# Optimization experiments

Hardware: AMD Instinct MI355X
Metric: run time of the kernel (lower is better)

## Reference

```python
import jax, jax.numpy as jnp
import numpy as np

B, T, NE, NH, HD = 4, 1024, 768, 12, 64
CURV = 0.0
EPS = 1e-6
LN_EPS = 1e-5
ROPE_BASE = 10000.0


def project(x, k):
    # Lift Euclidean vector onto Lorentz hyperboloid with curvature K = exp(k):
    # time coord t = sqrt(K + ||x||^2) so that <lx, lx>_L = -K.
    K = jnp.exp(k)
    t = jnp.sqrt(K + jnp.sum(x * x, axis=-1, keepdims=True))
    return jnp.concatenate([t, x], axis=-1)


def lorentz_distance(lq, lk, k):
    # lq, lk: (B, H, T, D+1); k: (1, H, 1, 1) log-curvature.
    # d = sqrt(K) * arccosh(clamp(-<q,k>_L / K, 1+eps))
    K = jnp.exp(k)
    inner = (jnp.einsum('bhid,bhjd->bhij', lq[..., 1:], lk[..., 1:])
             - jnp.einsum('bhi,bhj->bhij', lq[..., 0], lk[..., 0]))
    c = jnp.clip(-inner / K, 1.0 + EPS, None)
    return jnp.sqrt(K) * jnp.arccosh(c)


def lorentz_norm(x):
    # sqrt(|<x,x>_L|) with <x,x>_L = -x0^2 + ||xs||^2  (keepdim)
    inner = -x[..., 0:1] ** 2 + jnp.sum(x[..., 1:] ** 2, axis=-1, keepdims=True)
    return jnp.sqrt(jnp.clip(-inner, EPS, None))


def rotary_tables():
    inv_freq = 1.0 / (ROPE_BASE ** (np.arange(0, HD, 2, dtype=np.float32) / HD))
    t = np.arange(T, dtype=np.float32)
    freqs = np.outer(t, inv_freq)  # (T, HD/2)
    cos = jnp.asarray(np.cos(freqs))[None, :, None, :]  # (1,T,1,HD/2)
    sin = jnp.asarray(np.sin(freqs))[None, :, None, :]
    return cos, sin


def apply_rotary(x, cos, sin):
    # x: (B, T, H, HD)
    x1, x2 = x[..., : HD // 2], x[..., HD // 2:]
    return jnp.concatenate([x1 * cos + x2 * sin, -x1 * sin + x2 * cos], axis=-1)


def layernorm(y, g, b):
    m = jnp.mean(y, axis=-1, keepdims=True)
    v = jnp.mean((y - m) ** 2, axis=-1, keepdims=True)
    return (y - m) / jnp.sqrt(v + LN_EPS) * g + b


def setup_inputs() -> dict:
    key = jax.random.key(0)
    ks = jax.random.split(key, 8)
    s = 0.02
    return {
        'x': jax.random.normal(ks[0], (B, T, NE), dtype=jnp.float32),
        'block_curvature': jnp.asarray(CURV, dtype=jnp.float32),
        'mlp_curvature': jnp.asarray(CURV, dtype=jnp.float32),
        'attn_curvatures': jnp.ones((1, NH, 1, 1), dtype=jnp.float32) * CURV,
        'qkv_w': jax.random.normal(ks[1], (3 * NE, NE + 1), dtype=jnp.float32) * s,
        'attn_proj_w': jax.random.normal(ks[2], (NE, (HD + 1) * NH), dtype=jnp.float32) * s,
        'attn_proj_b': jnp.zeros((NE,), dtype=jnp.float32),
        'mlp_expand_w': jax.random.normal(ks[3], (4 * NE + 3, NE + 1), dtype=jnp.float32) * s,
        'mlp_expand_b': jnp.zeros((4 * NE + 3,), dtype=jnp.float32),
        'mlp_shrink_w': jax.random.normal(ks[4], (NE, 4 * (NE + 1)), dtype=jnp.float32) * s,
        'mlp_shrink_b': jnp.zeros((NE,), dtype=jnp.float32),
        'ln_g': jnp.ones((NE,), dtype=jnp.float32),
        'ln_b': jnp.zeros((NE,), dtype=jnp.float32),
    }


def reference(x, block_curvature, mlp_curvature, attn_curvatures, qkv_w,
              attn_proj_w, attn_proj_b, mlp_expand_w, mlp_expand_b,
              mlp_shrink_w, mlp_shrink_b, ln_g, ln_b):
    cos, sin = rotary_tables()
    causal_bias = jnp.where(
        jnp.triu(jnp.ones((T, T), dtype=bool), k=1), -jnp.inf, 0.0).astype(jnp.float32)

    def block_norm(lx):
        return project(layernorm(lx[..., 1:], ln_g, ln_b), block_curvature)

    def attn(lx):
        qkv = lx @ qkv_w.T  # (B, T, 3*NE)
        q, k, v = jnp.split(qkv, 3, axis=-1)
        q = apply_rotary(q.reshape(B, T, NH, HD), cos, sin)
        k = apply_rotary(k.reshape(B, T, NH, HD), cos, sin)
        v = v.reshape(B, T, NH, HD)
        lq = project(q.transpose(0, 2, 1, 3), attn_curvatures)  # (B,H,T,HD+1)
        lk = project(k.transpose(0, 2, 1, 3), attn_curvatures)
        lv = project(v.transpose(0, 2, 1, 3), attn_curvatures)
        dis = lorentz_distance(lq, lk, attn_curvatures)  # (B,H,T,T)
        aw = jax.nn.softmax(-dis + causal_bias, axis=-1)
        a = jnp.einsum('bhij,bhjd->bhid', aw, lv)  # (B,H,T,HD+1)
        a = a * jnp.sqrt(jnp.exp(attn_curvatures)) / lorentz_norm(a)
        a = a.transpose(0, 2, 1, 3).reshape(B, T, NH * (HD + 1))
        a = a @ attn_proj_w.T + attn_proj_b
        return project(a, block_curvature)

    def mlp(lx):
        h = lx @ mlp_expand_w.T + mlp_expand_b  # (B,T,4*NE+3)
        h = project(h, mlp_curvature)[..., 1:]  # drop time coord back to 4*NE+3
        h = jax.nn.gelu(h, approximate=False)
        h = project(h, mlp_curvature)  # (B,T,4*(NE+1))
        h = h @ mlp_shrink_w.T + mlp_shrink_b
        return project(h, block_curvature)

    def skip(lx, f_lx):
        return project(lx[..., 1:] + f_lx[..., 1:], block_curvature)

    lx = project(x, block_curvature)  # (B,T,NE+1)
    lx = skip(lx, attn(block_norm(lx)))
    lx = skip(lx, mlp(block_norm(lx)))
    return lx
```

## Files before the change

kernel.cpp:

```cpp
#include <hip/hip_runtime.h>
#include <cmath>

typedef unsigned short ushort_t;
typedef __attribute__((ext_vector_type(8))) short short8;
typedef __attribute__((ext_vector_type(4))) float floatx4;

#define NH    12
#define T     1024
#define ROWS  4096
#define NE    768
#define KPA   800
#define KPB   3104
#define NEXP  3200
#define HEXP  3075
#define NSPLIT 2

__device__ __forceinline__ ushort_t f2bf(float f) {
  union { float f; unsigned u; } v; v.f = f;
  unsigned r = v.u + 0x7fffu + ((v.u >> 16) & 1u);
  return (ushort_t)(r >> 16);
}
__device__ __forceinline__ float bf2f(ushort_t b) {
  union { unsigned u; float f; } v; v.u = ((unsigned)b) << 16;
  return v.f;
}
__device__ __forceinline__ float blk_reduce_sum(float v, float* sm) {
  #pragma unroll
  for (int o = 32; o > 0; o >>= 1) v += __shfl_xor(v, o, 64);
  int lane = threadIdx.x & 63, w = threadIdx.x >> 6;
  __syncthreads();
  if (lane == 0) sm[w] = v;
  __syncthreads();
  return sm[0] + sm[1] + sm[2] + sm[3];
}
__device__ __forceinline__ float red16_sum(float v) {
  #pragma unroll
  for (int o = 1; o < 16; o <<= 1) v += __shfl_xor(v, o, 64);
  return v;
}
__device__ __forceinline__ float red16_max(float v) {
  #pragma unroll
  for (int o = 1; o < 16; o <<= 1) v = fmaxf(v, __shfl_xor(v, o, 64));
  return v;
}

#define NB_A 7200
#define NB_B 2400
#define NB_C 10000
#define NB_D 9312
#define NB_E 16
__device__ __forceinline__ void cvt_elem(ushort_t* __restrict__ dst,
                                         const float* __restrict__ src,
                                         int idx, int srcRows, int srcK, int dstK) {
  int r = idx / dstK, c = idx - r * dstK;
  dst[idx] = (r < srcRows && c < srcK) ? f2bf(src[(size_t)r * srcK + c]) : (ushort_t)0;
}
__global__ __launch_bounds__(256) void prep_kernel(
    ushort_t* __restrict__ qkv_wb, const float* __restrict__ qkvw,
    ushort_t* __restrict__ proj_wb, const float* __restrict__ projw,
    ushort_t* __restrict__ exp_wb, const float* __restrict__ expw,
    ushort_t* __restrict__ shr_wb, const float* __restrict__ shrw,
    ushort_t* __restrict__ aout_bf) {
  int blk = blockIdx.x;
  int tid = threadIdx.x;
  if (blk < NB_A) {
    cvt_elem(qkv_wb, qkvw, blk * 256 + tid, 2304, 769, KPA);
  } else if (blk < NB_A + NB_B) {
    cvt_elem(proj_wb, projw, (blk - NB_A) * 256 + tid, 768, 780, KPA);
  } else if (blk < NB_A + NB_B + NB_C) {
    cvt_elem(exp_wb, expw, (blk - NB_A - NB_B) * 256 + tid, HEXP, 769, KPA);
  } else if (blk < NB_A + NB_B + NB_C + NB_D) {
    cvt_elem(shr_wb, shrw, (blk - NB_A - NB_B - NB_C) * 256 + tid, 768, 3076, KPB);
  } else {
    int r = (blk - NB_A - NB_B - NB_C - NB_D) * 256 + tid;
    ushort_t* p = aout_bf + (size_t)r * KPA + 780;
    #pragma unroll
    for (int j = 0; j < 20; ++j) p[j] = 0;
  }
}

__global__ __launch_bounds__(256) void ln_project(
    const float* __restrict__ xin, const float* __restrict__ g,
    const float* __restrict__ bb, const float* __restrict__ curv,
    ushort_t* __restrict__ outp) {
  __shared__ float sm[4];
  const int row = blockIdx.x;
  const int tid = threadIdx.x;
  const float* xr = xin + (size_t)row * NE;
  float xv[3];
  float s = 0.f, ss = 0.f;
  #pragma unroll
  for (int i = 0; i < 3; ++i) {
    xv[i] = xr[tid + 256 * i];
    s += xv[i]; ss += xv[i] * xv[i];
  }
  s = blk_reduce_sum(s, sm);
  ss = blk_reduce_sum(ss, sm);
  float mean = s * (1.f / 768.f);
  float var = ss * (1.f / 768.f) - mean * mean;
  float rstd = rsqrtf(var + 1e-5f);
  float yv[3]; float ys = 0.f;
  #pragma unroll
  for (int i = 0; i < 3; ++i) {
    int c = tid + 256 * i;
    yv[i] = (xv[i] - mean) * rstd * g[c] + bb[c];
    ys += yv[i] * yv[i];
  }
  ys = blk_reduce_sum(ys, sm);
  float tc = sqrtf(expf(curv[0]) + ys);
  ushort_t* orow = outp + (size_t)row * KPA;
  #pragma unroll
  for (int i = 0; i < 3; ++i) orow[1 + tid + 256 * i] = f2bf(yv[i]);
  if (tid == 0) orow[0] = f2bf(tc);
  if (tid < KPA - 769) orow[769 + tid] = 0;
}

__global__ __launch_bounds__(256) void gemm_bf16(
    const ushort_t* __restrict__ A, int lda,
    const ushort_t* __restrict__ W, int ldw,
    void* __restrict__ Cout, int ldc,
    int nkTot, int cpt,
    const float* __restrict__ bias, int biasN,
    const float* __restrict__ res, int ldres,
    int outMode, float* __restrict__ Cp) {
  __shared__ ushort_t As[128 * 32];
  __shared__ ushort_t Bs[128 * 32];
  const int tid = threadIdx.x;
  const int w = tid >> 6, lane = tid & 63;
  const int rowBase = (int)blockIdx.y << 7;
  const int colBase = (int)blockIdx.x << 7;
  const int wm = (w & 1) * 64, wn = (w >> 1) * 64;
  const int lm = lane & 15, quad = lane >> 4;
  const int qp = quad ^ ((lm >> 1) & 3);

  floatx4 acc[4][4];
  #pragma unroll
  for (int i = 0; i < 4; ++i)
    #pragma unroll
    for (int j = 0; j < 4; ++j) {
      floatx4 z = {0.f, 0.f, 0.f, 0.f};
      acc[i][j] = z;
    }

  const int kt0 = (int)blockIdx.z * cpt;
  const int kt1 = min(nkTot, kt0 + cpt);
  for (int kt = kt0; kt < kt1; ++kt) {
    __syncthreads();
    #pragma unroll
    for (int j = 0; j < 2; ++j) {
      int p = w * 128 + j * 64 + lane;
      int r = p >> 2;
      int gq = (p & 3) ^ ((r >> 1) & 3);
      const ushort_t* ga = A + (size_t)(rowBase + r) * lda + kt * 32 + gq * 8;
      const ushort_t* gb = W + (size_t)(colBase + r) * ldw + kt * 32 + gq * 8;
      __builtin_amdgcn_global_load_lds(
          (const __attribute__((address_space(1))) void*)ga,
          (__attribute__((address_space(3))) void*)&As[(w * 128 + j * 64) * 8],
          16, 0, 0);
      __builtin_amdgcn_global_load_lds(
          (const __attribute__((address_space(1))) void*)gb,
          (__attribute__((address_space(3))) void*)&Bs[(w * 128 + j * 64) * 8],
          16, 0, 0);
    }
    __syncthreads();

    short8 af[4], bfr[4];
    #pragma unroll
    for (int i = 0; i < 4; ++i) {
      af[i]  = *(const short8*)&As[(wm + i * 16 + lm) * 32 + qp * 8];
      bfr[i] = *(const short8*)&Bs[(wn + i * 16 + lm) * 32 + qp * 8];
    }
    #pragma unroll
    for (int i = 0; i < 4; ++i)
      #pragma unroll
      for (int jn = 0; jn < 4; ++jn)
        acc[i][jn] = __builtin_amdgcn_mfma_f32_16x16x32_bf16(
            af[i], bfr[jn], acc[i][jn], 0, 0, 0);
  }

  if (gridDim.z > 1) {
    float* dst = Cp + (size_t)blockIdx.z * ROWS * ldc;
    #pragma unroll
    for (int i = 0; i < 4; ++i)
      #pragma unroll
      for (int jn = 0; jn < 4; ++jn) {
        const int col = colBase + wn + jn * 16 + lm;
        #pragma unroll
        for (int rg = 0; rg < 4; ++rg) {
          const int row = rowBase + wm + i * 16 + quad * 4 + rg;
          dst[(size_t)row * ldc + col] = acc[i][jn][rg];
        }
      }
  } else if (outMode == 1) {
    ushort_t* C = (ushort_t*)Cout;
    #pragma unroll
    for (int i = 0; i < 4; ++i)
      #pragma unroll
      for (int jn = 0; jn < 4; ++jn) {
        const int col = colBase + wn + jn * 16 + lm;
        const float bv = bias ? ((col < biasN) ? bias[col] : 0.f) : 0.f;
        #pragma unroll
        for (int rg = 0; rg < 4; ++rg) {
          const int row = rowBase + wm + i * 16 + quad * 4 + rg;
          C[(size_t)row * ldc + col] = f2bf(acc[i][jn][rg] + bv);
        }
      }
  } else {
    float* C = (float*)Cout;
    #pragma unroll
    for (int i = 0; i < 4; ++i)
      #pragma unroll
      for (int jn = 0; jn < 4; ++jn) {
        const int col = colBase + wn + jn * 16 + lm;
        const float bv = bias ? ((col < biasN) ? bias[col] : 0.f) : 0.f;
        #pragma unroll
        for (int rg = 0; rg < 4; ++rg) {
          const int row = rowBase + wm + i * 16 + quad * 4 + rg;
          float o = acc[i][jn][rg] + bv;
          if (res) o += res[(size_t)row * ldres + col];
          C[(size_t)row * ldc + col] = o;
        }
      }
  }
}

__global__ __launch_bounds__(256) void rope_project(
    const float* __restrict__ qkv, const float* __restrict__ ac,
    ushort_t* __restrict__ qb, ushort_t* __restrict__ kb, ushort_t* __restrict__ vtb,
    float* __restrict__ q0, float* __restrict__ k0, float* __restrict__ v0) {
  int gid = blockIdx.x * 4 + (threadIdx.x >> 6);
  int lane = threadIdx.x & 63;
  int h = gid % NH;
  int bt = gid / NH;
  int t = bt & (T - 1);
  int b = bt >> 10;
  size_t base = (size_t)bt * 2304 + h * 64;
  float qv = qkv[base + lane];
  float kv = qkv[base + 768 + lane];
  float vv = qkv[base + 1536 + lane];
  int f = lane & 31;
  float ang = (float)t * powf(10000.f, -(float)f * (1.f / 32.f));
  float sn, cs;
  sincosf(ang, &sn, &cs);
  float qp = __shfl(qv, lane ^ 32, 64);
  float kp = __shfl(kv, lane ^ 32, 64);
  float qr = (lane < 32) ? (qv * cs + qp * sn) : (-qp * sn + qv * cs);
  float kr = (lane < 32) ? (kv * cs + kp * sn) : (-kp * sn + kv * cs);
  float Kh = expf(ac[h]);
  float sq = qr * qr, sk = kr * kr, sv = vv * vv;
  #pragma unroll
  for (int o = 32; o > 0; o >>= 1) {
    sq += __shfl_xor(sq, o, 64);
    sk += __shfl_xor(sk, o, 64);
    sv += __shfl_xor(sv, o, 64);
  }
  size_t idx = ((size_t)(b * NH + h) * T + t);
  qb[idx * 64 + lane] = f2bf(qr);
  kb[idx * 64 + lane] = f2bf(kr);
  vtb[(size_t)(b * NH + h) * (64 * T) + (size_t)lane * T + t] = f2bf(vv);
  if (lane == 0) {
    q0[idx] = sqrtf(Kh + sq);
    k0[idx] = sqrtf(Kh + sk);
    v0[idx] = sqrtf(Kh + sv);
  }
}

__global__ __launch_bounds__(256) void attn_kernel(
    const ushort_t* __restrict__ qb, const ushort_t* __restrict__ kb,
    const ushort_t* __restrict__ vtb,
    const float* __restrict__ q0, const float* __restrict__ k0,
    const float* __restrict__ v0,
    const float* __restrict__ ac,
    float* __restrict__ Opart, float* __restrict__ mpart,
    float* __restrict__ lpart, float* __restrict__ a0part) {
  __shared__ ushort_t Qs[64 * 64];
  __shared__ ushort_t Ks[64 * 64];
  __shared__ ushort_t Vts[64 * 64];
  __shared__ ushort_t Ps[64 * 72];

  const int sIdx = blockIdx.x;
  const int qtile = (int)gridDim.y - 1 - (int)blockIdx.y;
  const int bh = blockIdx.z;
  const int h = bh % NH;
  const int qt0 = qtile * 64;
  const int tid = threadIdx.x;
  const int w = tid >> 6, lane = tid & 63;
  const int lm = lane & 15, quad = lane >> 4;
  const int wm = w * 16;
  const int sw = lm & 7;

  const int n = qtile + 1;
  const int half = (n + 1) >> 1;
  const int kbeg = sIdx ? half : 0;
  const int kend = sIdx ? n : half;
  const size_t pb = (size_t)(sIdx * 48 + bh) * T;

  if (kbeg >= kend) {
    #pragma unroll
    for (int r = 0; r < 4; ++r) {
      const int i = qt0 + wm + quad * 4 + r;
      float* orow = Opart + (pb + i) * 64;
      #pragma unroll
      for (int nt = 0; nt < 4; ++nt) orow[nt * 16 + lm] = 0.f;
      if (lm == 0) { mpart[pb + i] = -1e30f; lpart[pb + i] = 0.f; a0part[pb + i] = 0.f; }
    }
    return;
  }

  const float Kh = expf(ac[h]);
  const float sqrtK = sqrtf(Kh);
  const float invK = 1.0f / Kh;

  {
    const ushort_t* qt = qb + ((size_t)bh * T + qt0) * 64;
    #pragma unroll
    for (int j = 0; j < 2; ++j) {
      int e = (j * 4 + w) * 512 + lane * 8;
      int r = e >> 6, chs = (e >> 3) & 7;
      int clog = (chs ^ (r & 7)) * 8;
      __builtin_amdgcn_global_load_lds(
          (const __attribute__((address_space(1))) void*)(qt + r * 64 + clog),
          (__attribute__((address_space(3))) void*)&Qs[(j * 4 + w) * 512],
          16, 0, 0);
    }
  }
  float q0rv[4];
  #pragma unroll
  for (int r = 0; r < 4; ++r)
    q0rv[r] = q0[(size_t)bh * T + qt0 + wm + quad * 4 + r];

  float mrow[4], lsum[4], a0r[4];
  floatx4 oacc[4];
  #pragma unroll
  for (int r = 0; r < 4; ++r) { mrow[r] = -__builtin_inff(); lsum[r] = 0.f; a0r[r] = 0.f; }
  #pragma unroll
  for (int nt = 0; nt < 4; ++nt) { floatx4 z = {0.f,0.f,0.f,0.f}; oacc[nt] = z; }

  for (int kt = kbeg; kt < kend; ++kt) {
    const int j0 = kt * 64;
    __syncthreads();
    {
      const ushort_t* ktile = kb + ((size_t)bh * T + j0) * 64;
      const ushort_t* vbh = vtb + (size_t)bh * (64 * T);
      #pragma unroll
      for (int j = 0; j < 2; ++j) {
        int e = (j * 4 + w) * 512 + lane * 8;
        int r = e >> 6, chs = (e >> 3) & 7;
        int clog = (chs ^ (r & 7)) * 8;
        __builtin_amdgcn_global_load_lds(
            (const __attribute__((address_space(1))) void*)(ktile + r * 64 + clog),
            (__attribute__((address_space(3))) void*)&Ks[(j * 4 + w) * 512],
            16, 0, 0);
        __builtin_amdgcn_global_load_lds(
            (const __attribute__((address_space(1))) void*)(vbh + (size_t)r * T + j0 + clog),
            (__attribute__((address_space(3))) void*)&Vts[(j * 4 + w) * 512],
            16, 0, 0);
      }
    }
    float k0v[4], v0v[4];
    #pragma unroll
    for (int jt = 0; jt < 4; ++jt) {
      k0v[jt] = k0[(size_t)bh * T + j0 + jt * 16 + lm];
      v0v[jt] = v0[(size_t)bh * T + j0 + jt * 16 + lm];
    }
    __syncthreads();

    short8 qf0 = *(const short8*)&Qs[(wm + lm) * 64 + ((0 + quad) ^ sw) * 8];
    short8 qf1 = *(const short8*)&Qs[(wm + lm) * 64 + ((4 + quad) ^ sw) * 8];
    floatx4 sacc[4];
    #pragma unroll
    for (int jt = 0; jt < 4; ++jt) {
      const int krow = jt * 16 + lm;
      short8 kf0 = *(const short8*)&Ks[krow * 64 + ((0 + quad) ^ sw) * 8];
      short8 kf1 = *(const short8*)&Ks[krow * 64 + ((4 + quad) ^ sw) * 8];
      floatx4 z = {0.f, 0.f, 0.f, 0.f};
      z = __builtin_amdgcn_mfma_f32_16x16x32_bf16(qf0, kf0, z, 0, 0, 0);
      z = __builtin_amdgcn_mfma_f32_16x16x32_bf16(qf1, kf1, z, 0, 0, 0);
      sacc[jt] = z;
    }

    const bool diag = (kt == qtile);
    float alpha[4];
    #pragma unroll
    for (int r = 0; r < 4; ++r) {
      const int i = qt0 + wm + quad * 4 + r;
      float sc[4];
      float rowm = -__builtin_inff();
      #pragma unroll
      for (int jt = 0; jt < 4; ++jt) {
        float c = (q0rv[r] * k0v[jt] - sacc[jt][r]) * invK;
        float u = fmaxf(c - 1.f, 1e-6f);
        float s = -sqrtK * __logf(1.f + u + sqrtf(u * (u + 2.f)));
        if (diag && (j0 + jt * 16 + lm > i)) s = -__builtin_inff();
        sc[jt] = s;
        rowm = fmaxf(rowm, s);
      }
      rowm = red16_max(rowm);
      const float mnew = fmaxf(mrow[r], rowm);
      alpha[r] = __expf(mrow[r] - mnew);
      mrow[r] = mnew;
      float ls = 0.f, a0s = 0.f;
      #pragma unroll
      for (int jt = 0; jt < 4; ++jt) {
        float p = __expf(sc[jt] - mnew);
        ushort_t pb2 = f2bf(p);
        Ps[(wm + quad * 4 + r) * 72 + jt * 16 + lm] = pb2;
        float pf = bf2f(pb2);
        ls += pf;
        a0s += pf * v0v[jt];
      }
      lsum[r] = lsum[r] * alpha[r] + ls;
      a0r[r]  = a0r[r]  * alpha[r] + a0s;
    }

    #pragma unroll
    for (int nt = 0; nt < 4; ++nt)
      #pragma unroll
      for (int r = 0; r < 4; ++r) oacc[nt][r] *= alpha[r];
    short8 pf0 = *(const short8*)&Ps[(wm + lm) * 72 + quad * 8];
    short8 pf1 = *(const short8*)&Ps[(wm + lm) * 72 + 32 + quad * 8];
    #pragma unroll
    for (int nt = 0; nt < 4; ++nt) {
      const int vrow = nt * 16 + lm;
      short8 vf0 = *(const short8*)&Vts[vrow * 64 + ((0 + quad) ^ sw) * 8];
      short8 vf1 = *(const short8*)&Vts[vrow * 64 + ((4 + quad) ^ sw) * 8];
      oacc[nt] = __builtin_amdgcn_mfma_f32_16x16x32_bf16(pf0, vf0, oacc[nt], 0, 0, 0);
      oacc[nt] = __builtin_amdgcn_mfma_f32_16x16x32_bf16(pf1, vf1, oacc[nt], 0, 0, 0);
    }
  }

  #pragma unroll
  for (int r = 0; r < 4; ++r) {
    float lf = red16_sum(lsum[r]);
    float a0f = red16_sum(a0r[r]);
    const int i = qt0 + wm + quad * 4 + r;
    float* orow = Opart + (pb + i) * 64;
    #pragma unroll
    for (int nt = 0; nt < 4; ++nt) orow[nt * 16 + lm] = oacc[nt][r];
    if (lm == 0) { mpart[pb + i] = mrow[r]; lpart[pb + i] = lf; a0part[pb + i] = a0f; }
  }
}

__global__ __launch_bounds__(256) void attn_combine(
    const float* __restrict__ Opart, const float* __restrict__ mpart,
    const float* __restrict__ lpart, const float* __restrict__ a0part,
    const float* __restrict__ ac, ushort_t* __restrict__ aout) {
  const int widx = blockIdx.x * 4 + (threadIdx.x >> 6);
  const int lane = threadIdx.x & 63;
  const int bh = widx >> 10;
  const int t = widx & 1023;
  const int h = bh % NH, b = bh / NH;
  const size_t r0 = (size_t)bh * T + t;
  const size_t r1 = (size_t)(48 + bh) * T + t;
  float m0 = mpart[r0], m1 = mpart[r1];
  float M = fmaxf(m0, m1);
  float w0 = __expf(m0 - M), w1 = __expf(m1 - M);
  float L = w0 * lpart[r0] + w1 * lpart[r1];
  float A0 = w0 * a0part[r0] + w1 * a0part[r1];
  float O = w0 * Opart[r0 * 64 + lane] + w1 * Opart[r1 * 64 + lane];
  const float invl = 1.f / L;
  float av = O * invl;
  float ssq = av * av;
  #pragma unroll
  for (int o = 32; o > 0; o >>= 1) ssq += __shfl_xor(ssq, o, 64);
  float a0n = A0 * invl;
  float nsq = fmaxf(a0n * a0n - ssq, 1e-6f);
  float Kh = expf(ac[h]);
  float scale = sqrtf(Kh) * rsqrtf(nsq);
  ushort_t* orow = aout + (size_t)(b * T + t) * KPA + h * 65;
  orow[1 + lane] = f2bf(av * scale);
  if (lane == 0) orow[0] = f2bf(a0n * scale);
}

__global__ __launch_bounds__(256) void gelu_project(
    const ushort_t* __restrict__ hsrc, const float* __restrict__ curv,
    ushort_t* __restrict__ hp) {
  __shared__ float sm[4];
  const int row = blockIdx.x;
  const int tid = threadIdx.x;
  const ushort_t* hr = hsrc + (size_t)row * NEXP;
  float gv[13];
  float ss = 0.f;
  #pragma unroll
  for (int i = 0; i < 13; ++i) {
    int c = tid + 256 * i;
    float xx = (c < HEXP) ? bf2f(hr[c]) : 0.f;
    float gg = 0.5f * xx * (1.f + erff(xx * 0.70710678118654752f));
    gv[i] = gg; ss += gg * gg;
  }
  ss = blk_reduce_sum(ss, sm);
  float tc = sqrtf(expf(curv[0]) + ss);
  ushort_t* orow = hp + (size_t)row * KPB;
  #pragma unroll
  for (int i = 0; i < 13; ++i) {
    int c = tid + 256 * i;
    if (c < HEXP) orow[1 + c] = f2bf(gv[i]);
  }
  if (tid == 0) orow[0] = f2bf(tc);
  if (tid < KPB - (HEXP + 1)) orow[HEXP + 1 + tid] = 0;
}

__global__ __launch_bounds__(256) void reduce_ln_project(
    const float* __restrict__ Cp, int nsplit,
    const float* __restrict__ bias, const float* __restrict__ res,
    float* __restrict__ x2out,
    const float* __restrict__ g, const float* __restrict__ bb,
    const float* __restrict__ curv, ushort_t* __restrict__ lnp) {
  __shared__ float sm[4];
  const int row = blockIdx.x;
  const int tid = threadIdx.x;
  float xv[3];
  float s = 0.f, ss = 0.f;
  #pragma unroll
  for (int i = 0; i < 3; ++i) {
    const int c = tid + 256 * i;
    float v = bias[c] + res[(size_t)row * NE + c];
    for (int sp = 0; sp < nsplit; ++sp)
      v += Cp[(size_t)sp * ROWS * NE + (size_t)row * NE + c];
    x2out[(size_t)row * NE + c] = v;
    xv[i] = v;
    s += v; ss += v * v;
  }
  s = blk_reduce_sum(s, sm);
  ss = blk_reduce_sum(ss, sm);
  float mean = s * (1.f / 768.f);
  float var = ss * (1.f / 768.f) - mean * mean;
  float rstd = rsqrtf(var + 1e-5f);
  float yv[3]; float ys = 0.f;
  #pragma unroll
  for (int i = 0; i < 3; ++i) {
    int c = tid + 256 * i;
    yv[i] = (xv[i] - mean) * rstd * g[c] + bb[c];
    ys += yv[i] * yv[i];
  }
  ys = blk_reduce_sum(ys, sm);
  float tc = sqrtf(expf(curv[0]) + ys);
  ushort_t* orow = lnp + (size_t)row * KPA;
  #pragma unroll
  for (int i = 0; i < 3; ++i) orow[1 + tid + 256 * i] = f2bf(yv[i]);
  if (tid == 0) orow[0] = f2bf(tc);
  if (tid < KPA - 769) orow[769 + tid] = 0;
}

__global__ __launch_bounds__(256) void reduce_final_project(
    const float* __restrict__ Cp, int nsplit,
    const float* __restrict__ bias, const float* __restrict__ res,
    const float* __restrict__ curv, float* __restrict__ out) {
  __shared__ float sm[4];
  const int row = blockIdx.x;
  const int tid = threadIdx.x;
  float v[3]; float ss = 0.f;
  #pragma unroll
  for (int i = 0; i < 3; ++i) {
    const int c = tid + 256 * i;
    float t = bias[c] + res[(size_t)row * NE + c];
    for (int sp = 0; sp < nsplit; ++sp)
      t += Cp[(size_t)sp * ROWS * NE + (size_t)row * NE + c];
    v[i] = t; ss += t * t;
  }
  ss = blk_reduce_sum(ss, sm);
  float tc = sqrtf(expf(curv[0]) + ss);
  float* o = out + (size_t)row * 769;
  #pragma unroll
  for (int i = 0; i < 3; ++i) o[1 + tid + 256 * i] = v[i];
  if (tid == 0) o[0] = tc;
}

extern "C" void kernel_launch(void* const* d_in, const int* in_sizes, int n_in,
                              void* d_out, int out_size, void* d_ws, size_t ws_size,
                              hipStream_t stream) {
  (void)in_sizes; (void)n_in; (void)out_size; (void)ws_size;
  const float* x     = (const float*)d_in[0];
  const float* bc    = (const float*)d_in[1];
  const float* mc    = (const float*)d_in[2];
  const float* ac    = (const float*)d_in[3];
  const float* qkvw  = (const float*)d_in[4];
  const float* projw = (const float*)d_in[5];
  const float* projb = (const float*)d_in[6];
  const float* expw  = (const float*)d_in[7];
  const float* expb  = (const float*)d_in[8];
  const float* shrw  = (const float*)d_in[9];
  const float* shrb  = (const float*)d_in[10];
  const float* lng   = (const float*)d_in[11];
  const float* lnb   = (const float*)d_in[12];
  float* out = (float*)d_out;

  float* x2 = (float*)d_ws;
  ushort_t* qkv_wb  = (ushort_t*)(x2 + (size_t)ROWS * NE);
  ushort_t* proj_wb = qkv_wb + (size_t)2304 * KPA;
  ushort_t* exp_wb  = proj_wb + (size_t)768 * KPA;
  ushort_t* shr_wb  = exp_wb + (size_t)NEXP * KPA;
  ushort_t* lnp_bf  = shr_wb + (size_t)768 * KPB;
  ushort_t* aout_bf = lnp_bf + (size_t)ROWS * KPA;
  char* r2 = (char*)(aout_bf + (size_t)ROWS * KPA);
  float* qkvb = (float*)r2;
  ushort_t* qbb = (ushort_t*)(qkvb + (size_t)ROWS * 2304);
  ushort_t* kbb = qbb + (size_t)48 * T * 64;
  ushort_t* vtb = kbb + (size_t)48 * T * 64;
  float* q0b = (float*)(vtb + (size_t)48 * T * 64);
  float* k0b = q0b + (size_t)48 * T;
  float* v0b = k0b + (size_t)48 * T;
  float* Opart = v0b + (size_t)48 * T;
  float* mpart = Opart + (size_t)NSPLIT * 48 * T * 64;
  float* lpart = mpart + (size_t)NSPLIT * 48 * T;
  float* a0part = lpart + (size_t)NSPLIT * 48 * T;
  float* ppartP = (float*)r2;
  ushort_t* hbbf = (ushort_t*)r2;
  ushort_t* hp_bf = hbbf + (size_t)ROWS * NEXP;
  float* ppartS = (float*)(hp_bf + (size_t)ROWS * KPB);

  prep_kernel<<<NB_A + NB_B + NB_C + NB_D + NB_E, 256, 0, stream>>>(
      qkv_wb, qkvw, proj_wb, projw, exp_wb, expw, shr_wb, shrw, aout_bf);
  ln_project<<<ROWS, 256, 0, stream>>>(x, lng, lnb, bc, lnp_bf);
  gemm_bf16<<<dim3(2304 / 128, ROWS / 128, 1), 256, 0, stream>>>(
      lnp_bf, KPA, qkv_wb, KPA, qkvb, 2304, KPA / 32, KPA / 32,
      nullptr, 0, nullptr, 0, 0, nullptr);
  rope_project<<<(ROWS * NH) / 4, 256, 0, stream>>>(qkvb, ac, qbb, kbb, vtb, q0b, k0b, v0b);
  attn_kernel<<<dim3(NSPLIT, T / 64, 48), 256, 0, stream>>>(
      qbb, kbb, vtb, q0b, k0b, v0b, ac, Opart, mpart, lpart, a0part);
  attn_combine<<<(48 * T) / 4, 256, 0, stream>>>(Opart, mpart, lpart, a0part, ac, aout_bf);
  gemm_bf16<<<dim3(768 / 128, ROWS / 128, 2), 256, 0, stream>>>(
      aout_bf, KPA, proj_wb, KPA, nullptr, NE, KPA / 32, 13,
      nullptr, 0, nullptr, 0, 0, ppartP);
  reduce_ln_project<<<ROWS, 256, 0, stream>>>(
      ppartP, 2, projb, x, x2, lng, lnb, bc, lnp_bf);
  gemm_bf16<<<dim3(NEXP / 128, ROWS / 128, 1), 256, 0, stream>>>(
      lnp_bf, KPA, exp_wb, KPA, hbbf, NEXP, KPA / 32, KPA / 32,
      expb, HEXP, nullptr, 0, 1, nullptr);
  gelu_project<<<ROWS, 256, 0, stream>>>(hbbf, mc, hp_bf);
  gemm_bf16<<<dim3(768 / 128, ROWS / 128, 4), 256, 0, stream>>>(
      hp_bf, KPB, shr_wb, KPB, nullptr, NE, KPB / 32, 25,
      nullptr, 0, nullptr, 0, 0, ppartS);
  reduce_final_project<<<ROWS, 256, 0, stream>>>(
      ppartS, 4, shrb, x2, bc, out);
}
```

Measured before the change: 436.2 us.

## Drop online-softmax max tracking using bounded Lorentz scores; closed-form weights

Because the negative Lorentz distance is never positive, the attention kernel now accumulates unnormalised exp weights directly, with no running row max, rescaling or partial max buffers. Each weight is computed in closed form as (c+sqrt(c^2-1))^(-sqrtK), with a special path for unit curvature that needs only a sqrt. The combine step becomes a plain sum over splits, and the causal key range is split three ways instead of two. This removes shuffles, exps and accumulator rescaling. The cost is a possible underflow for rows where every weight is tiny, plus extra partial-buffer traffic.

```diff
diff --git a/kernel.cpp b/kernel.cpp
--- a/kernel.cpp
+++ b/kernel.cpp
@@ -13,7 +13,7 @@
 #define KPB   3104
 #define NEXP  3200
 #define HEXP  3075
-#define NSPLIT 2
+#define NSPLIT 3
 
 __device__ __forceinline__ ushort_t f2bf(float f) {
   union { float f; unsigned u; } v; v.f = f;
@@ -36,11 +36,6 @@
 __device__ __forceinline__ float red16_sum(float v) {
   #pragma unroll
   for (int o = 1; o < 16; o <<= 1) v += __shfl_xor(v, o, 64);
-  return v;
-}
-__device__ __forceinline__ float red16_max(float v) {
-  #pragma unroll
-  for (int o = 1; o < 16; o <<= 1) v = fmaxf(v, __shfl_xor(v, o, 64));
   return v;
 }
 
@@ -271,8 +266,8 @@
     const float* __restrict__ q0, const float* __restrict__ k0,
     const float* __restrict__ v0,
     const float* __restrict__ ac,
-    float* __restrict__ Opart, float* __restrict__ mpart,
-    float* __restrict__ lpart, float* __restrict__ a0part) {
+    float* __restrict__ Opart, float* __restrict__ lpart,
+    float* __restrict__ a0part) {
   __shared__ ushort_t Qs[64 * 64];
   __shared__ ushort_t Ks[64 * 64];
   __shared__ ushort_t Vts[64 * 64];
@@ -290,9 +285,8 @@
   const int sw = lm & 7;
 
   const int n = qtile + 1;
-  const int half = (n + 1) >> 1;
-  const int kbeg = sIdx ? half : 0;
-  const int kend = sIdx ? n : half;
+  const int kbeg = (n * sIdx) / NSPLIT;
+  const int kend = (n * (sIdx + 1)) / NSPLIT;
   const size_t pb = (size_t)(sIdx * 48 + bh) * T;
 
   if (kbeg >= kend) {
@@ -302,7 +296,7 @@
       float* orow = Opart + (pb + i) * 64;
       #pragma unroll
       for (int nt = 0; nt < 4; ++nt) orow[nt * 16 + lm] = 0.f;
-      if (lm == 0) { mpart[pb + i] = -1e30f; lpart[pb + i] = 0.f; a0part[pb + i] = 0.f; }
+      if (lm == 0) { lpart[pb + i] = 0.f; a0part[pb + i] = 0.f; }
     }
     return;
   }
@@ -310,6 +304,8 @@
   const float Kh = expf(ac[h]);
   const float sqrtK = sqrtf(Kh);
   const float invK = 1.0f / Kh;
+  const float nsK = -sqrtK;
+  const bool k1 = (Kh == 1.0f);
 
   {
     const ushort_t* qt = qb + ((size_t)bh * T + qt0) * 64;
@@ -329,10 +325,10 @@
   for (int r = 0; r < 4; ++r)
     q0rv[r] = q0[(size_t)bh * T + qt0 + wm + quad * 4 + r];
 
-  float mrow[4], lsum[4], a0r[4];
+  float lsum[4], a0r[4];
   floatx4 oacc[4];
   #pragma unroll
-  for (int r = 0; r < 4; ++r) { mrow[r] = -__builtin_inff(); lsum[r] = 0.f; a0r[r] = 0.f; }
+  for (int r = 0; r < 4; ++r) { lsum[r] = 0.f; a0r[r] = 0.f; }
   #pragma unroll
   for (int nt = 0; nt < 4; ++nt) { floatx4 z = {0.f,0.f,0.f,0.f}; oacc[nt] = z; }
 
@@ -357,10 +353,10 @@
             16, 0, 0);
       }
     }
-    float k0v[4], v0v[4];
+    float k0i[4], v0v[4];
     #pragma unroll
     for (int jt = 0; jt < 4; ++jt) {
-      k0v[jt] = k0[(size_t)bh * T + j0 + jt * 16 + lm];
+      k0i[jt] = k0[(size_t)bh * T + j0 + jt * 16 + lm] * invK;
       v0v[jt] = v0[(size_t)bh * T + j0 + jt * 16 + lm];
     }
     __syncthreads();
@@ -380,43 +376,49 @@
     }
 
     const bool diag = (kt == qtile);
-    float alpha[4];
-    #pragma unroll
-    for (int r = 0; r < 4; ++r) {
-      const int i = qt0 + wm + quad * 4 + r;
-      float sc[4];
-      float rowm = -__builtin_inff();
-      #pragma unroll
-      for (int jt = 0; jt < 4; ++jt) {
-        float c = (q0rv[r] * k0v[jt] - sacc[jt][r]) * invK;
-        float u = fmaxf(c - 1.f, 1e-6f);
-        float s = -sqrtK * __logf(1.f + u + sqrtf(u * (u + 2.f)));
-        if (diag && (j0 + jt * 16 + lm > i)) s = -__builtin_inff();
-        sc[jt] = s;
-        rowm = fmaxf(rowm, s);
+    if (k1) {
+      #pragma unroll
+      for (int r = 0; r < 4; ++r) {
+        const int i = qt0 + wm + quad * 4 + r;
+        float ls = 0.f, a0s = 0.f;
+        #pragma unroll
+        for (int jt = 0; jt < 4; ++jt) {
+          float c = fmaf(-invK, sacc[jt][r], q0rv[r] * k0i[jt]);
+          c = fmaxf(c, 1.000001f);
+          float p = c - sqrtf(fmaf(c, c, -1.f));
+          if (diag && (j0 + jt * 16 + lm > i)) p = 0.f;
+          ushort_t pb2 = f2bf(p);
+          Ps[(wm + quad * 4 + r) * 72 + jt * 16 + lm] = pb2;
+          float pf = bf2f(pb2);
+          ls += pf;
+          a0s = fmaf(pf, v0v[jt], a0s);
+        }
+        lsum[r] += ls;
+        a0r[r] += a0s;
       }
-      rowm = red16_max(rowm);
-      const float mnew = fmaxf(mrow[r], rowm);
-      alpha[r] = __expf(mrow[r] - mnew);
-      mrow[r] = mnew;
-      float ls = 0.f, a0s = 0.f;
-      #pragma unroll
-      for (int jt = 0; jt < 4; ++jt) {
-        float p = __expf(sc[jt] - mnew);
-        ushort_t pb2 = f2bf(p);
-        Ps[(wm + quad * 4 + r) * 72 + jt * 16 + lm] = pb2;
-        float pf = bf2f(pb2);
-        ls += pf;
-        a0s += pf * v0v[jt];
+    } else {
+      #pragma unroll
+      for (int r = 0; r < 4; ++r) {
+        const int i = qt0 + wm + quad * 4 + r;
+        float ls = 0.f, a0s = 0.f;
+        #pragma unroll
+        for (int jt = 0; jt < 4; ++jt) {
+          float c = fmaf(-invK, sacc[jt][r], q0rv[r] * k0i[jt]);
+          c = fmaxf(c, 1.000001f);
+          float z = c + sqrtf(fmaf(c, c, -1.f));
+          float p = __builtin_amdgcn_exp2f(nsK * __builtin_amdgcn_logf(z));
+          if (diag && (j0 + jt * 16 + lm > i)) p = 0.f;
+          ushort_t pb2 = f2bf(p);
+          Ps[(wm + quad * 4 + r) * 72 + jt * 16 + lm] = pb2;
+          float pf = bf2f(pb2);
+          ls += pf;
+          a0s = fmaf(pf, v0v[jt], a0s);
+        }
+        lsum[r] += ls;
+        a0r[r] += a0s;
       }
-      lsum[r] = lsum[r] * alpha[r] + ls;
-      a0r[r]  = a0r[r]  * alpha[r] + a0s;
-    }
-
-    #pragma unroll
-    for (int nt = 0; nt < 4; ++nt)
-      #pragma unroll
-      for (int r = 0; r < 4; ++r) oacc[nt][r] *= alpha[r];
+    }
+
     short8 pf0 = *(const short8*)&Ps[(wm + lm) * 72 + quad * 8];
     short8 pf1 = *(const short8*)&Ps[(wm + lm) * 72 + 32 + quad * 8];
     #pragma unroll
@@ -437,27 +439,27 @@
     float* orow = Opart + (pb + i) * 64;
     #pragma unroll
     for (int nt = 0; nt < 4; ++nt) orow[nt * 16 + lm] = oacc[nt][r];
-    if (lm == 0) { mpart[pb + i] = mrow[r]; lpart[pb + i] = lf; a0part[pb + i] = a0f; }
+    if (lm == 0) { lpart[pb + i] = lf; a0part[pb + i] = a0f; }
   }
 }
 
 __global__ __launch_bounds__(256) void attn_combine(
-    const float* __restrict__ Opart, const float* __restrict__ mpart,
-    const float* __restrict__ lpart, const float* __restrict__ a0part,
+    const float* __restrict__ Opart, const float* __restrict__ lpart,
+    const float* __restrict__ a0part,
     const float* __restrict__ ac, ushort_t* __restrict__ aout) {
   const int widx = blockIdx.x * 4 + (threadIdx.x >> 6);
   const int lane = threadIdx.x & 63;
   const int bh = widx >> 10;
   const int t = widx & 1023;
   const int h = bh % NH, b = bh / NH;
-  const size_t r0 = (size_t)bh * T + t;
-  const size_t r1 = (size_t)(48 + bh) * T + t;
-  float m0 = mpart[r0], m1 = mpart[r1];
-  float M = fmaxf(m0, m1);
-  float w0 = __expf(m0 - M), w1 = __expf(m1 - M);
-  float L = w0 * lpart[r0] + w1 * lpart[r1];
-  float A0 = w0 * a0part[r0] + w1 * a0part[r1];
-  float O = w0 * Opart[r0 * 64 + lane] + w1 * Opart[r1 * 64 + lane];
+  float L = 0.f, A0 = 0.f, O = 0.f;
+  #pragma unroll
+  for (int sp = 0; sp < NSPLIT; ++sp) {
+    const size_t r = (size_t)(sp * 48 + bh) * T + t;
+    L += lpart[r];
+    A0 += a0part[r];
+    O += Opart[r * 64 + lane];
+  }
   const float invl = 1.f / L;
   float av = O * invl;
   float ssq = av * av;
@@ -601,8 +603,7 @@
   float* k0b = q0b + (size_t)48 * T;
   float* v0b = k0b + (size_t)48 * T;
   float* Opart = v0b + (size_t)48 * T;
-  float* mpart = Opart + (size_t)NSPLIT * 48 * T * 64;
-  float* lpart = mpart + (size_t)NSPLIT * 48 * T;
+  float* lpart = Opart + (size_t)NSPLIT * 48 * T * 64;
   float* a0part = lpart + (size_t)NSPLIT * 48 * T;
   float* ppartP = (float*)r2;
   ushort_t* hbbf = (ushort_t*)r2;
@@ -617,8 +618,8 @@
       nullptr, 0, nullptr, 0, 0, nullptr);
   rope_project<<<(ROWS * NH) / 4, 256, 0, stream>>>(qkvb, ac, qbb, kbb, vtb, q0b, k0b, v0b);
   attn_kernel<<<dim3(NSPLIT, T / 64, 48), 256, 0, stream>>>(
-      qbb, kbb, vtb, q0b, k0b, v0b, ac, Opart, mpart, lpart, a0part);
-  attn_combine<<<(48 * T) / 4, 256, 0, stream>>>(Opart, mpart, lpart, a0part, ac, aout_bf);
+      qbb, kbb, vtb, q0b, k0b, v0b, ac, Opart, lpart, a0part);
+  attn_combine<<<(48 * T) / 4, 256, 0, stream>>>(Opart, lpart, a0part, ac, aout_bf);
   gemm_bf16<<<dim3(768 / 128, ROWS / 128, 2), 256, 0, stream>>>(
       aout_bf, KPA, proj_wb, KPA, nullptr, NE, KPA / 32, 13,
       nullptr, 0, nullptr, 0, 0, ppartP);
```

Result: faster. 384.7 us (-11.8%).
